# Kernel optimization log

Hardware: AMD Instinct MI355X
Metric: run time of the kernel (lower is better)

The kernel has to match this reference:

```python
import jax, jax.numpy as jnp
import numpy as np

V, E, H = 32000, 128, 128

def setup_inputs() -> dict:
    key = jax.random.key(0)
    ks = jax.random.split(key, 12)
    s = 0.05
    x = jax.random.randint(ks[0], (256, 512), 0, V)
    emb = jax.random.normal(ks[1], (V, E), jnp.float32) * s
    Wi = jax.random.normal(ks[2], (E + H, H), jnp.float32) * s
    bi = jnp.zeros((H,), jnp.float32)
    Wf = jax.random.normal(ks[3], (E + H, H), jnp.float32) * s
    bf = jnp.zeros((H,), jnp.float32)
    Wc = jax.random.normal(ks[4], (E + H, H), jnp.float32) * s
    bc = jnp.zeros((H,), jnp.float32)
    Wo = jax.random.normal(ks[5], (E + H, H), jnp.float32) * s
    bo = jnp.zeros((H,), jnp.float32)
    Wout = jax.random.normal(ks[6], (H, V), jnp.float32) * s
    bout = jnp.zeros((V,), jnp.float32)
    return {"x": x, "emb": emb, "Wi": Wi, "bi": bi, "Wf": Wf, "bf": bf,
            "Wc": Wc, "bc": bc, "Wo": Wo, "bo": bo, "Wout": Wout, "bout": bout}

def reference(x, emb, Wi, bi, Wf, bf, Wc, bc, Wo, bo, Wout, bout):
    B, T = x.shape
    xe = emb[x]                       # [B, T, E] embedding gather
    xe_t = jnp.swapaxes(xe, 0, 1)     # [T, B, E] for scan over time

    def step(carry, e_t):
        h, c = carry
        comb = jnp.concatenate([e_t, h], axis=1)          # [B, E+H]
        f = jax.nn.sigmoid(comb @ Wf + bf)
        i = jax.nn.sigmoid(comb @ Wi + bi)
        o = jax.nn.sigmoid(comb @ Wo + bo)
        c_ = jnp.tanh(comb @ Wc + bc)
        c = f * c + i * c_
        h = o * jnp.tanh(c)
        return (h, c), None

    h0 = jnp.zeros((B, H), xe.dtype)
    c0 = jnp.zeros((B, H), xe.dtype)
    (h, _), _ = jax.lax.scan(step, (h0, c0), xe_t)
    return h @ Wout + bout            # [B, V] logits from final hidden state
```

## Files before the change

### kernel.cpp

```cpp
#include <hip/hip_runtime.h>

constexpr int TT = 512;
constexpr int BB = 256;
constexpr int HH = 128;
constexpr int VV = 32000;

typedef _Float16 h2 __attribute__((ext_vector_type(2)));
typedef _Float16 f16x4 __attribute__((ext_vector_type(4)));
typedef _Float16 f16x8 __attribute__((ext_vector_type(8)));
typedef float f32x4 __attribute__((ext_vector_type(4)));

struct __align__(16) H2x4 { h2 a, b, c, d; };

__device__ __forceinline__ h2 pkrtz(float a, float b) {
  return __builtin_bit_cast(h2, __builtin_amdgcn_cvt_pkrtz(a, b));
}
__device__ __forceinline__ float fdot2(h2 a, h2 b, float c) {
  return __builtin_amdgcn_fdot2(a, b, c, false);
}
template <int CTRL>
__device__ __forceinline__ float qmov(float v) {
  return __builtin_bit_cast(
      float, __builtin_amdgcn_mov_dpp(__builtin_bit_cast(int, v), CTRL, 0xf,
                                      0xf, true));
}

__global__ __launch_bounds__(256, 4) void wprep(
    const float* __restrict__ Wi, const float* __restrict__ bi,
    const float* __restrict__ Wf, const float* __restrict__ bf,
    const float* __restrict__ Wc, const float* __restrict__ bc,
    const float* __restrict__ Wo, const float* __restrict__ bo,
    _Float16* __restrict__ Wct, float* __restrict__ bcat) {
  const int n = blockIdx.x;
  const int g = n & 3;
  const int u = n >> 2;
  const float* Wg = (g == 0) ? Wi : (g == 1) ? Wf : (g == 2) ? Wc : Wo;
  const float* bg = (g == 0) ? bi : (g == 1) ? bf : (g == 2) ? bc : bo;
  const int k = threadIdx.x;
  Wct[(size_t)n * 256 + k] = (_Float16)Wg[(size_t)k * HH + u];
  if (k == 0) bcat[n] = bg[u];
}

__global__ __launch_bounds__(512, 2) void lstm_rec(
    const int* __restrict__ x, const float* __restrict__ emb,
    const _Float16* __restrict__ Wct, const float* __restrict__ bcat,
    _Float16* __restrict__ hbf) {
  const int b = blockIdx.x;
  const int tid = threadIdx.x;
  const int w = tid >> 6;
  const int l = tid & 63;
  const int qk = l & 3;
  const int u = 16 * w + (l >> 2);
  const int n16 = l & 15;
  const int quad = l >> 4;

  __shared__ int xrow[TT];
  __shared__ __align__(16) _Float16 comb[2][HH];
  __shared__ __align__(16) _Float16 xch[64][514];

  xrow[tid] = x[(size_t)b * TT + tid];
  if (tid < HH) comb[0][tid] = (_Float16)0.f;

  h2 wr2[4][16];
#pragma unroll
  for (int g = 0; g < 4; ++g) {
    const _Float16* wp = Wct + (size_t)(4 * u + g) * 256 + 128 + 32 * qk;
#pragma unroll
    for (int j = 0; j < 4; ++j) {
      const H2x4 q = __builtin_bit_cast(H2x4, *(const f16x8*)(wp + 8 * j));
      wr2[g][4 * j + 0] = q.a;
      wr2[g][4 * j + 1] = q.b;
      wr2[g][4 * j + 2] = q.c;
      wr2[g][4 * j + 3] = q.d;
    }
  }

  f16x8 wfx[4][4];
  f32x4 biasr[4];
#pragma unroll
  for (int nt = 0; nt < 4; ++nt) {
#pragma unroll
    for (int ks = 0; ks < 4; ++ks)
      wfx[nt][ks] = *(const f16x8*)(Wct +
                                    (size_t)(64 * w + nt * 16 + n16) * 256 +
                                    ks * 32 + quad * 8);
    biasr[nt] = *(const f32x4*)(bcat + 64 * w + nt * 16 + quad * 4);
  }

  const bool isc = (qk == 2);
  const float k1 = isc ? 2.f : -1.f;
  const float gam = isc ? -2.f : 1.f;
  const float del = isc ? 1.f : 0.f;

  float cst = 0.f;
  float hv = 0.f;
  int buf = 0;

  __syncthreads();

  for (int c = 0; c < 8; ++c) {
#pragma unroll 2
    for (int tt = 0; tt < 4; ++tt) {
      const int vid = xrow[c * 64 + tt * 16 + n16];
      const float* ep = emb + (size_t)vid * HH + quad * 8;
      f16x8 ef[4];
#pragma unroll
      for (int ks = 0; ks < 4; ++ks) {
        const float4 e0 = *(const float4*)(ep + ks * 32);
        const float4 e1 = *(const float4*)(ep + ks * 32 + 4);
        H2x4 q;
        q.a = pkrtz(e0.x, e0.y);
        q.b = pkrtz(e0.z, e0.w);
        q.c = pkrtz(e1.x, e1.y);
        q.d = pkrtz(e1.z, e1.w);
        ef[ks] = __builtin_bit_cast(f16x8, q);
      }
      f32x4 acc[4] = {};
#pragma unroll
      for (int ks = 0; ks < 4; ++ks)
#pragma unroll
        for (int nt = 0; nt < 4; ++nt)
          acc[nt] = __builtin_amdgcn_mfma_f32_16x16x32_f16(wfx[nt][ks], ef[ks],
                                                           acc[nt], 0, 0, 0);
#pragma unroll
      for (int nt = 0; nt < 4; ++nt) {
        const f32x4 av = acc[nt] + biasr[nt];
        _Float16* dst = &xch[tt * 16 + n16][64 * w + nt * 16 + quad * 4];
        *(h2*)dst = pkrtz(av[0], av[1]);
        *(h2*)(dst + 2) = pkrtz(av[2], av[3]);
      }
    }
    __syncthreads();

#pragma unroll 2
    for (int tl = 0; tl < 64; ++tl) {
      const float xev = (float)xch[tl][tid];
      const _Float16* cb = &comb[buf][32 * qk];
      const H2x4 q0 = __builtin_bit_cast(H2x4, *(const f16x8*)(cb));
      const H2x4 q1 = __builtin_bit_cast(H2x4, *(const f16x8*)(cb + 8));
      const H2x4 q2 = __builtin_bit_cast(H2x4, *(const f16x8*)(cb + 16));
      const H2x4 q3 = __builtin_bit_cast(H2x4, *(const f16x8*)(cb + 24));
      float s0 = 0.f, s1 = 0.f, s2 = 0.f, s3 = 0.f;
#define DOT16(sg, g)                  \
  sg = fdot2(q0.a, wr2[g][0], sg);    \
  sg = fdot2(q0.b, wr2[g][1], sg);    \
  sg = fdot2(q0.c, wr2[g][2], sg);    \
  sg = fdot2(q0.d, wr2[g][3], sg);    \
  sg = fdot2(q1.a, wr2[g][4], sg);    \
  sg = fdot2(q1.b, wr2[g][5], sg);    \
  sg = fdot2(q1.c, wr2[g][6], sg);    \
  sg = fdot2(q1.d, wr2[g][7], sg);    \
  sg = fdot2(q2.a, wr2[g][8], sg);    \
  sg = fdot2(q2.b, wr2[g][9], sg);    \
  sg = fdot2(q2.c, wr2[g][10], sg);   \
  sg = fdot2(q2.d, wr2[g][11], sg);   \
  sg = fdot2(q3.a, wr2[g][12], sg);   \
  sg = fdot2(q3.b, wr2[g][13], sg);   \
  sg = fdot2(q3.c, wr2[g][14], sg);   \
  sg = fdot2(q3.d, wr2[g][15], sg);
      DOT16(s0, 0)
      DOT16(s1, 1)
      DOT16(s2, 2)
      DOT16(s3, 3)
#undef DOT16
      s0 += qmov<0xB1>(s0);
      s1 += qmov<0xB1>(s1);
      s2 += qmov<0xB1>(s2);
      s3 += qmov<0xB1>(s3);
      s0 += qmov<0x4E>(s0);
      s1 += qmov<0x4E>(s1);
      s2 += qmov<0x4E>(s2);
      s3 += qmov<0x4E>(s3);
      const float aown =
          (qk == 0 ? s0 : qk == 1 ? s1 : qk == 2 ? s2 : s3) + xev;
      const float ex = __expf(k1 * aown);
      const float act = gam / (1.f + ex) + del;
      const float ax1 = qmov<0xB1>(act);
      const float va = (qk & 1) ? ax1 : act;
      const float vb = (qk & 1) ? act : ax1;
      const float vax = qmov<0x4E>(va);
      const float vbx = qmov<0x4E>(vb);
      const float gi = (qk & 2) ? vax : va;
      const float gf = (qk & 2) ? vbx : vb;
      const float gc = (qk & 2) ? va : vax;
      const float go = (qk & 2) ? vb : vbx;
      cst = gf * cst + gi * gc;
      const float th = 1.f - 2.f / (__expf(2.f * cst) + 1.f);
      hv = go * th;
      if (qk == 0) comb[buf ^ 1][u] = (_Float16)hv;
      __syncthreads();
      buf ^= 1;
    }
  }
  if (qk == 0) hbf[(size_t)b * HH + u] = (_Float16)hv;
}

__global__ __launch_bounds__(256, 4) void wout_tr(const float* __restrict__ Wout,
                                                  _Float16* __restrict__ Wt) {
  const int v = blockIdx.x * 256 + threadIdx.x;
#pragma unroll 1
  for (int kc = 0; kc < 16; ++kc) {
    float f[8];
#pragma unroll
    for (int i = 0; i < 8; ++i) f[i] = Wout[(size_t)(kc * 8 + i) * VV + v];
    H2x4 q;
    q.a = pkrtz(f[0], f[1]);
    q.b = pkrtz(f[2], f[3]);
    q.c = pkrtz(f[4], f[5]);
    q.d = pkrtz(f[6], f[7]);
    *(H2x4*)(Wt + (size_t)v * HH + kc * 8) = q;
  }
}

__global__ __launch_bounds__(256, 4) void lstm_out(
    const _Float16* __restrict__ Wt, const _Float16* __restrict__ hbf,
    const float* __restrict__ bout, float* __restrict__ out) {
  const int tid = threadIdx.x;
  const int wv = tid >> 6;
  const int lane = tid & 63;
  const int vblk = blockIdx.x % 250;
  const int batblk = blockIdx.x / 250;
  const int n16 = lane & 15;
  const int quad = lane >> 4;
  const int vbase = vblk * 128 + wv * 32;
  const int batbase = batblk * 64;

  f32x4 acc[4][2] = {};
#pragma unroll
  for (int ks = 0; ks < 4; ++ks) {
    const int k = ks * 32 + quad * 8;
    f16x8 a[4], bf_[2];
#pragma unroll
    for (int mt = 0; mt < 4; ++mt)
      a[mt] = *(const f16x8*)(hbf + (size_t)(batbase + mt * 16 + n16) * HH + k);
#pragma unroll
    for (int vt = 0; vt < 2; ++vt)
      bf_[vt] = *(const f16x8*)(Wt + (size_t)(vbase + vt * 16 + n16) * HH + k);
#pragma unroll
    for (int mt = 0; mt < 4; ++mt)
#pragma unroll
      for (int vt = 0; vt < 2; ++vt)
        acc[mt][vt] = __builtin_amdgcn_mfma_f32_16x16x32_f16(a[mt], bf_[vt],
                                                             acc[mt][vt], 0, 0, 0);
  }
#pragma unroll
  for (int vt = 0; vt < 2; ++vt) {
    const int v = vbase + vt * 16 + n16;
    const float bv = bout[v];
#pragma unroll
    for (int mt = 0; mt < 4; ++mt) {
#pragma unroll
      for (int r = 0; r < 4; ++r) {
        const int bat = batbase + mt * 16 + quad * 4 + r;
        out[(size_t)bat * VV + v] = acc[mt][vt][r] + bv;
      }
    }
  }
}

extern "C" void kernel_launch(void* const* d_in, const int* in_sizes, int n_in,
                              void* d_out, int out_size, void* d_ws,
                              size_t ws_size, hipStream_t stream) {
  const int* x = (const int*)d_in[0];
  const float* emb = (const float*)d_in[1];
  const float* Wi = (const float*)d_in[2];
  const float* bi = (const float*)d_in[3];
  const float* Wf = (const float*)d_in[4];
  const float* bf = (const float*)d_in[5];
  const float* Wc = (const float*)d_in[6];
  const float* bc = (const float*)d_in[7];
  const float* Wo = (const float*)d_in[8];
  const float* bo = (const float*)d_in[9];
  const float* Wout = (const float*)d_in[10];
  const float* bout = (const float*)d_in[11];
  float* out = (float*)d_out;

  _Float16* Wt = (_Float16*)d_ws;
  _Float16* hbf = Wt + (size_t)VV * HH;
  _Float16* Wct = hbf + (size_t)BB * HH;
  float* bcat = (float*)(Wct + 512 * 256);

  wprep<<<512, 256, 0, stream>>>(Wi, bi, Wf, bf, Wc, bc, Wo, bo, Wct, bcat);
  wout_tr<<<VV / 256, 256, 0, stream>>>(Wout, Wt);
  lstm_rec<<<BB, 512, 0, stream>>>(x, emb, Wct, bcat, hbf);
  lstm_out<<<(VV / 128) * (BB / 64), 256, 0, stream>>>(Wt, hbf, bout, out);
}
```

Baseline: 480.3 us.

## Use MFMA for recurrent h·W matvec and fold activation scales into weights

Replaces the per-step fdot2 plus DPP-reduction recurrent matvec with 16x16x32 f16 MFMA instructions, holding the hidden-weight fragments in registers and broadcasting h as the B operand. The lane-to-unit mapping changes so each lane reads all four gate pre-activations for one unit straight from the MFMA accumulator layout, which removes the cross-lane shuffles. The log2e and tanh scale factors are folded into the weights and biases at prep time so the gates need only exp2 and rcp intrinsics. The cost is redundant MFMA work, since batch is one column per block and 15 of 16 columns are wasted, plus lower-precision rcp/exp approximations.

Result: faster. 426.2 us (-11.3%).

```diff
diff --git a/kernel.cpp b/kernel.cpp
--- a/kernel.cpp
+++ b/kernel.cpp
@@ -15,15 +15,15 @@
 __device__ __forceinline__ h2 pkrtz(float a, float b) {
   return __builtin_bit_cast(h2, __builtin_amdgcn_cvt_pkrtz(a, b));
 }
-__device__ __forceinline__ float fdot2(h2 a, h2 b, float c) {
-  return __builtin_amdgcn_fdot2(a, b, c, false);
-}
-template <int CTRL>
-__device__ __forceinline__ float qmov(float v) {
-  return __builtin_bit_cast(
-      float, __builtin_amdgcn_mov_dpp(__builtin_bit_cast(int, v), CTRL, 0xf,
-                                      0xf, true));
-}
+__device__ __forceinline__ float fexp2(float x) {
+  return __builtin_amdgcn_exp2f(x);
+}
+__device__ __forceinline__ float frcp(float x) {
+  return __builtin_amdgcn_rcpf(x);
+}
+
+constexpr float SC_SIG = -1.4426950408889634f;
+constexpr float SC_TANH = 2.8853900817779268f;
 
 __global__ __launch_bounds__(256, 4) void wprep(
     const float* __restrict__ Wi, const float* __restrict__ bi,
@@ -36,9 +36,10 @@
   const int u = n >> 2;
   const float* Wg = (g == 0) ? Wi : (g == 1) ? Wf : (g == 2) ? Wc : Wo;
   const float* bg = (g == 0) ? bi : (g == 1) ? bf : (g == 2) ? bc : bo;
+  const float sc = (g == 2) ? SC_TANH : SC_SIG;
   const int k = threadIdx.x;
-  Wct[(size_t)n * 256 + k] = (_Float16)Wg[(size_t)k * HH + u];
-  if (k == 0) bcat[n] = bg[u];
+  Wct[(size_t)n * 256 + k] = (_Float16)(Wg[(size_t)k * HH + u] * sc);
+  if (k == 0) bcat[n] = bg[u] * sc;
 }
 
 __global__ __launch_bounds__(512, 2) void lstm_rec(
@@ -49,31 +50,26 @@
   const int tid = threadIdx.x;
   const int w = tid >> 6;
   const int l = tid & 63;
-  const int qk = l & 3;
-  const int u = 16 * w + (l >> 2);
   const int n16 = l & 15;
   const int quad = l >> 4;
+  const int nts = n16 & 3;
+  const int u = 16 * w + 4 * nts + quad;
 
   __shared__ int xrow[TT];
   __shared__ __align__(16) _Float16 comb[2][HH];
-  __shared__ __align__(16) _Float16 xch[64][514];
+  __shared__ __align__(16) _Float16 xch[64][516];
 
   xrow[tid] = x[(size_t)b * TT + tid];
   if (tid < HH) comb[0][tid] = (_Float16)0.f;
 
-  h2 wr2[4][16];
-#pragma unroll
-  for (int g = 0; g < 4; ++g) {
-    const _Float16* wp = Wct + (size_t)(4 * u + g) * 256 + 128 + 32 * qk;
-#pragma unroll
-    for (int j = 0; j < 4; ++j) {
-      const H2x4 q = __builtin_bit_cast(H2x4, *(const f16x8*)(wp + 8 * j));
-      wr2[g][4 * j + 0] = q.a;
-      wr2[g][4 * j + 1] = q.b;
-      wr2[g][4 * j + 2] = q.c;
-      wr2[g][4 * j + 3] = q.d;
-    }
-  }
+  f16x8 wh[4][4];
+#pragma unroll
+  for (int nt = 0; nt < 4; ++nt)
+#pragma unroll
+    for (int ks = 0; ks < 4; ++ks)
+      wh[nt][ks] = *(const f16x8*)(Wct +
+                                   (size_t)(64 * w + nt * 16 + n16) * 256 +
+                                   128 + ks * 32 + quad * 8);
 
   f16x8 wfx[4][4];
   f32x4 biasr[4];
@@ -86,11 +82,6 @@
                                     ks * 32 + quad * 8);
     biasr[nt] = *(const f32x4*)(bcat + 64 * w + nt * 16 + quad * 4);
   }
-
-  const bool isc = (qk == 2);
-  const float k1 = isc ? 2.f : -1.f;
-  const float gam = isc ? -2.f : 1.f;
-  const float del = isc ? 1.f : 0.f;
 
   float cst = 0.f;
   float hv = 0.f;
@@ -134,65 +125,51 @@
 
 #pragma unroll 2
     for (int tl = 0; tl < 64; ++tl) {
-      const float xev = (float)xch[tl][tid];
-      const _Float16* cb = &comb[buf][32 * qk];
-      const H2x4 q0 = __builtin_bit_cast(H2x4, *(const f16x8*)(cb));
-      const H2x4 q1 = __builtin_bit_cast(H2x4, *(const f16x8*)(cb + 8));
-      const H2x4 q2 = __builtin_bit_cast(H2x4, *(const f16x8*)(cb + 16));
-      const H2x4 q3 = __builtin_bit_cast(H2x4, *(const f16x8*)(cb + 24));
-      float s0 = 0.f, s1 = 0.f, s2 = 0.f, s3 = 0.f;
-#define DOT16(sg, g)                  \
-  sg = fdot2(q0.a, wr2[g][0], sg);    \
-  sg = fdot2(q0.b, wr2[g][1], sg);    \
-  sg = fdot2(q0.c, wr2[g][2], sg);    \
-  sg = fdot2(q0.d, wr2[g][3], sg);    \
-  sg = fdot2(q1.a, wr2[g][4], sg);    \
-  sg = fdot2(q1.b, wr2[g][5], sg);    \
-  sg = fdot2(q1.c, wr2[g][6], sg);    \
-  sg = fdot2(q1.d, wr2[g][7], sg);    \
-  sg = fdot2(q2.a, wr2[g][8], sg);    \
-  sg = fdot2(q2.b, wr2[g][9], sg);    \
-  sg = fdot2(q2.c, wr2[g][10], sg);   \
-  sg = fdot2(q2.d, wr2[g][11], sg);   \
-  sg = fdot2(q3.a, wr2[g][12], sg);   \
-  sg = fdot2(q3.b, wr2[g][13], sg);   \
-  sg = fdot2(q3.c, wr2[g][14], sg);   \
-  sg = fdot2(q3.d, wr2[g][15], sg);
-      DOT16(s0, 0)
-      DOT16(s1, 1)
-      DOT16(s2, 2)
-      DOT16(s3, 3)
-#undef DOT16
-      s0 += qmov<0xB1>(s0);
-      s1 += qmov<0xB1>(s1);
-      s2 += qmov<0xB1>(s2);
-      s3 += qmov<0xB1>(s3);
-      s0 += qmov<0x4E>(s0);
-      s1 += qmov<0x4E>(s1);
-      s2 += qmov<0x4E>(s2);
-      s3 += qmov<0x4E>(s3);
-      const float aown =
-          (qk == 0 ? s0 : qk == 1 ? s1 : qk == 2 ? s2 : s3) + xev;
-      const float ex = __expf(k1 * aown);
-      const float act = gam / (1.f + ex) + del;
-      const float ax1 = qmov<0xB1>(act);
-      const float va = (qk & 1) ? ax1 : act;
-      const float vb = (qk & 1) ? act : ax1;
-      const float vax = qmov<0x4E>(va);
-      const float vbx = qmov<0x4E>(vb);
-      const float gi = (qk & 2) ? vax : va;
-      const float gf = (qk & 2) ? vbx : vb;
-      const float gc = (qk & 2) ? va : vax;
-      const float go = (qk & 2) ? vb : vbx;
+      const f16x4 xe4 = *(const f16x4*)(&xch[tl][4 * u]);
+
+      const _Float16* cb = comb[buf];
+      f16x8 hb[4];
+#pragma unroll
+      for (int ks = 0; ks < 4; ++ks)
+        hb[ks] = *(const f16x8*)(cb + ks * 32 + quad * 8);
+
+      f32x4 acc[4] = {};
+#pragma unroll
+      for (int ks = 0; ks < 4; ++ks)
+#pragma unroll
+        for (int nt = 0; nt < 4; ++nt)
+          acc[nt] = __builtin_amdgcn_mfma_f32_16x16x32_f16(wh[nt][ks], hb[ks],
+                                                           acc[nt], 0, 0, 0);
+
+      const bool s1 = (n16 & 1) != 0;
+      const bool s2 = (n16 & 2) != 0;
+      const f32x4 t01 = s1 ? acc[1] : acc[0];
+      const f32x4 t23 = s1 ? acc[3] : acc[2];
+      const f32x4 av = s2 ? t23 : t01;
+
+      const float a0 = av[0] + (float)xe4[0];
+      const float a1 = av[1] + (float)xe4[1];
+      const float a2 = av[2] + (float)xe4[2];
+      const float a3 = av[3] + (float)xe4[3];
+
+      const float ei = fexp2(a0);
+      const float ef_ = fexp2(a1);
+      const float ec = fexp2(a2);
+      const float eo = fexp2(a3);
+      const float gi = frcp(1.f + ei);
+      const float gf = frcp(1.f + ef_);
+      const float gc = 1.f - 2.f * frcp(1.f + ec);
+      const float go = frcp(1.f + eo);
       cst = gf * cst + gi * gc;
-      const float th = 1.f - 2.f / (__expf(2.f * cst) + 1.f);
+      const float th = 1.f - 2.f * frcp(1.f + fexp2(cst * SC_TANH));
       hv = go * th;
-      if (qk == 0) comb[buf ^ 1][u] = (_Float16)hv;
+
+      if (n16 < 4) comb[buf ^ 1][u] = (_Float16)hv;
       __syncthreads();
       buf ^= 1;
     }
   }
-  if (qk == 0) hbf[(size_t)b * HH + u] = (_Float16)hv;
+  if (n16 < 4) hbf[(size_t)b * HH + u] = (_Float16)hv;
 }
 
 __global__ __launch_bounds__(256, 4) void wout_tr(const float* __restrict__ Wout,
```
